# Kernel optimization log

Hardware: AMD Instinct MI355X
Metric: run time of the kernel (lower is better)

## Reference

```python
import math
import jax, jax.numpy as jnp
import numpy as np

B, T, D, NH = 4, 2048, 1024, 16
HS = D // NH
N_BUCKETS = 32
MAX_DIST = 128


def _relative_position_bucket(rp):
    # bidirectional T5 bucketing, n_buckets=32, max_distance=128
    nb = N_BUCKETS // 2  # 16
    buckets = (rp > 0).astype(jnp.int32) * nb
    rp = jnp.abs(rp)
    max_exact = nb // 2  # 8
    is_small = rp < max_exact
    me = max_exact - 1   # 7
    nbm = nb - 1         # 15
    rp_safe = jnp.maximum(rp, 1).astype(jnp.float32)
    rp_large = me + (jnp.log(rp_safe / me) / math.log(MAX_DIST / me) * (nbm - me)).astype(jnp.int32)
    rp_large = jnp.minimum(rp_large, nbm)
    buckets = buckets + jnp.where(is_small, rp, rp_large)
    return buckets


def compute_bias(rel_emb, qT, kT):
    ctx = jnp.arange(qT, dtype=jnp.int32)[:, None]
    mem = jnp.arange(kT, dtype=jnp.int32)[None, :]
    bucket = _relative_position_bucket(mem - ctx)  # [qT, kT]
    values = rel_emb[bucket]                        # [qT, kT, NH]
    return jnp.transpose(values, (2, 0, 1))[None]   # [1, NH, qT, kT]


def setup_inputs() -> dict:
    key = jax.random.key(0)
    ks = jax.random.split(key, 6)
    s = 0.02
    return {
        "queries": jax.random.normal(ks[0], (B, T, D), jnp.float32),
        "Wq": jax.random.normal(ks[1], (D, D), jnp.float32) * s,
        "Wk": jax.random.normal(ks[2], (D, D), jnp.float32) * s,
        "Wv": jax.random.normal(ks[3], (D, D), jnp.float32) * s,
        "Wo": jax.random.normal(ks[4], (D, D), jnp.float32) * s,
        "rel_emb": jax.random.normal(ks[5], (N_BUCKETS, NH), jnp.float32) * s,
    }


def reference(queries, Wq, Wk, Wv, Wo, rel_emb):
    b, t, d = queries.shape
    def split_heads(x):
        return jnp.transpose(x.reshape(b, t, NH, HS), (0, 2, 1, 3))  # [B, nh, T, hs]
    q = split_heads(queries @ Wq.T)
    k = split_heads(queries @ Wk.T)
    v = split_heads(queries @ Wv.T)
    att = jnp.einsum('bhqd,bhkd->bhqk', q, k) * (1.0 / math.sqrt(HS))
    att = att + compute_bias(rel_emb, t, t)
    att = jax.nn.softmax(att, axis=-1)
    o = jnp.einsum('bhqk,bhkd->bhqd', att, v)
    o = jnp.transpose(o, (0, 2, 1, 3)).reshape(b, t, d)
    return o @ Wo.T
```

## Files before the change

kernel.cpp:

```cpp
#include <hip/hip_runtime.h>

#define T_SEQ 2048
#define D_MODEL 1024
#define NHEADS 16
#define HSZ 64
#define BATCH 4

typedef __bf16 bf16x8 __attribute__((ext_vector_type(8)));
typedef float f32x4 __attribute__((ext_vector_type(4)));

__device__ __forceinline__ unsigned short f2bf(float f) {
    unsigned int u = __builtin_bit_cast(unsigned int, f);
    u += 0x7fff + ((u >> 16) & 1);
    return (unsigned short)(u >> 16);
}

__device__ __forceinline__ unsigned int pk2bf(float a, float b) {
#if __has_builtin(__builtin_amdgcn_cvt_pk_bf16_f32)
    typedef __bf16 bf16x2_t __attribute__((ext_vector_type(2)));
    bf16x2_t v = __builtin_amdgcn_cvt_pk_bf16_f32(a, b);
    return __builtin_bit_cast(unsigned int, v);
#else
    return (unsigned int)f2bf(a) | ((unsigned int)f2bf(b) << 16);
#endif
}

__device__ __forceinline__ void gld_lds16(const void* g, void* lds) {
    __builtin_amdgcn_global_load_lds(
        (const __attribute__((address_space(1))) unsigned int*)g,
        (__attribute__((address_space(3))) unsigned int*)lds, 16, 0, 0);
}

__device__ __forceinline__ bf16x8 ld8(const unsigned short* p) {
    return *(const bf16x8*)p;
}

__global__ void cast_x(const float* __restrict__ src, unsigned short* __restrict__ dst, int n4) {
    int i = blockIdx.x * blockDim.x + threadIdx.x;
    if (i >= n4) return;
    float4 v = ((const float4*)src)[i];
    ushort4 o;
    o.x = f2bf(v.x); o.y = f2bf(v.y); o.z = f2bf(v.z); o.w = f2bf(v.w);
    ((ushort4*)dst)[i] = o;
}

__global__ void cast_w(const float* __restrict__ w0, const float* __restrict__ w1,
                       const float* __restrict__ w2, const float* __restrict__ w3,
                       unsigned short* __restrict__ dst) {
    const float* srcs[4] = {w0, w1, w2, w3};
    int wsel = blockIdx.y;
    const float4* src = (const float4*)srcs[wsel];
    int i = blockIdx.x * blockDim.x + threadIdx.x;
    float4 v = src[i];
    ushort4 o;
    o.x = f2bf(v.x); o.y = f2bf(v.y); o.z = f2bf(v.z); o.w = f2bf(v.w);
    ((ushort4*)(dst + (size_t)wsel * 1048576))[i] = o;
}

__global__ void bias_table(const float* __restrict__ rel_emb, float* __restrict__ bias_tab) {
    int idx = blockIdx.x * blockDim.x + threadIdx.x;
    if (idx >= NHEADS * 4095) return;
    int h = idx / 4095;
    int rp = (idx % 4095) - 2047;
    int bucket = rp > 0 ? 16 : 0;
    int arp = rp < 0 ? -rp : rp;
    if (arp < 8) {
        bucket += arp;
    } else {
        float f = logf((float)arp / 7.0f) * (8.0f / logf(128.0f / 7.0f));
        int rl = 7 + (int)f;
        bucket += rl < 15 ? rl : 15;
    }
    bias_tab[idx] = rel_emb[bucket * NHEADS + h] * 1.4426950408889634f;
}

template<int MODE>
__global__ __launch_bounds__(256, 2) void gemm_bt(
    const unsigned short* __restrict__ A,
    const unsigned short* __restrict__ Bw,
    void* __restrict__ out)
{
    constexpr int K = 1024;
    __shared__ unsigned short As[128 * 64];
    __shared__ unsigned short Bs[128 * 64];

    const int tid  = threadIdx.x;
    const int wave = tid >> 6;
    const int lane = tid & 63;
    const int quad = lane >> 4;
    const int l16  = lane & 15;
    const int wm   = wave >> 1;
    const int wn   = wave & 1;
    const int bn   = blockIdx.x;
    const int bm   = blockIdx.y;

    const int r_in = lane >> 3;
    const int lc   = (lane & 7) ^ r_in;

    f32x4 acc[4][4];
    #pragma unroll
    for (int m = 0; m < 4; ++m)
        #pragma unroll
        for (int n = 0; n < 4; ++n)
            acc[m][n] = f32x4{0.f, 0.f, 0.f, 0.f};

    const long a_row0 = (long)bm * 128;
    const long b_row0 = (long)bn * 128;

    for (int kt = 0; kt < K / 64; ++kt) {
        __syncthreads();
        const int k0 = kt * 64 + lc * 8;
        #pragma unroll
        for (int c = 0; c < 4; ++c) {
            int cc = wave * 4 + c;
            int r  = cc * 8 + r_in;
            gld_lds16(A  + (a_row0 + r) * K + k0, &As[cc * 512]);
            gld_lds16(Bw + (b_row0 + r) * K + k0, &Bs[cc * 512]);
        }
        __syncthreads();

        bf16x8 af[4][2], bf[4][2];
        #pragma unroll
        for (int m = 0; m < 4; ++m)
            #pragma unroll
            for (int ks = 0; ks < 2; ++ks) {
                int r  = wm * 64 + m * 16 + l16;
                int pc = (ks * 4 + quad) ^ (r & 7);
                af[m][ks] = ld8(&As[r * 64 + pc * 8]);
            }
        #pragma unroll
        for (int n = 0; n < 4; ++n)
            #pragma unroll
            for (int ks = 0; ks < 2; ++ks) {
                int r  = wn * 64 + n * 16 + l16;
                int pc = (ks * 4 + quad) ^ (r & 7);
                bf[n][ks] = ld8(&Bs[r * 64 + pc * 8]);
            }
        #pragma unroll
        for (int ks = 0; ks < 2; ++ks)
            #pragma unroll
            for (int m = 0; m < 4; ++m)
                #pragma unroll
                for (int n = 0; n < 4; ++n)
                    acc[m][n] = __builtin_amdgcn_mfma_f32_16x16x32_bf16(
                        af[m][ks], bf[n][ks], acc[m][n], 0, 0, 0);
    }

    const int which = (MODE == 4) ? (bn >> 3) : 0;
    #pragma unroll
    for (int m = 0; m < 4; ++m) {
        int row = bm * 128 + wm * 64 + m * 16 + quad * 4;
        #pragma unroll
        for (int n = 0; n < 4; ++n) {
            int col = bn * 128 + wn * 64 + n * 16 + l16;
            if (MODE == 3) {
                float* O = (float*)out;
                #pragma unroll
                for (int r = 0; r < 4; ++r)
                    O[(long)(row + r) * 1024 + col] = acc[m][n][r];
            } else {
                int cl = col & 1023;
                int h = cl >> 6, hs = cl & 63;
                int b = row >> 11, t = row & 2047;
                unsigned short* O = (unsigned short*)out + (size_t)which * 8388608;
                if (which == 2) {
                    ushort4 pk;
                    pk.x = f2bf(acc[m][n][0]); pk.y = f2bf(acc[m][n][1]);
                    pk.z = f2bf(acc[m][n][2]); pk.w = f2bf(acc[m][n][3]);
                    *(ushort4*)&O[(long)((b * 16 + h) * 64 + hs) * 2048 + t] = pk;
                } else {
                    #pragma unroll
                    for (int r = 0; r < 4; ++r) {
                        float v = acc[m][n][r];
                        if (which == 0) v *= 0.125f * 1.4426950408889634f;
                        O[(long)((b * 16 + h) * 2048 + (t + r)) * 64 + hs] = f2bf(v);
                    }
                }
            }
        }
    }
}

__global__ __launch_bounds__(256, 2) void attn(
    const unsigned short* __restrict__ Q,
    const unsigned short* __restrict__ Kb,
    const unsigned short* __restrict__ Vt,
    const float* __restrict__ bias_tab,
    unsigned short* __restrict__ AO)
{
    __shared__ unsigned short Ks[64 * 64];
    __shared__ unsigned short Vs[64 * 64];
    __shared__ unsigned short Ps[256 * 72];
    __shared__ float Bb[2303];

    const int tid  = threadIdx.x;
    const int wave = tid >> 6;
    const int lane = tid & 63;
    const int quad = lane >> 4;
    const int l16  = lane & 15;

    const int bh = blockIdx.y;
    const int b  = bh >> 4, h = bh & 15;
    const int q0 = blockIdx.x * 256;

    const unsigned short* Qg = Q  + (long)bh * T_SEQ * HSZ;
    const unsigned short* Kg = Kb + (long)bh * T_SEQ * HSZ;
    const unsigned short* Vg = Vt + (long)bh * HSZ * T_SEQ;

    {
        const float* bt = bias_tab + h * 4095 + (1792 - q0);
        for (int i = tid; i < 2303; i += 256) Bb[i] = bt[i];
    }

    bf16x8 qf[4][2];
    #pragma unroll
    for (int m = 0; m < 4; ++m)
        #pragma unroll
        for (int ks = 0; ks < 2; ++ks) {
            int t = q0 + wave * 64 + m * 16 + l16;
            qf[m][ks] = ld8(&Qg[(long)t * 64 + ks * 32 + quad * 8]);
        }

    f32x4 o[4][4];
    float li[4][4];
    #pragma unroll
    for (int m = 0; m < 4; ++m) {
        #pragma unroll
        for (int n = 0; n < 4; ++n) o[m][n] = f32x4{0.f, 0.f, 0.f, 0.f};
        #pragma unroll
        for (int r = 0; r < 4; ++r) li[m][r] = 0.0f;
    }

    const int r_in = lane >> 3;
    const int lc   = (lane & 7) ^ r_in;

    for (int kt = 0; kt < T_SEQ / 64; ++kt) {
        __syncthreads();
        #pragma unroll
        for (int c = 0; c < 2; ++c) {
            int cc = wave * 2 + c;
            int r  = cc * 8 + r_in;
            gld_lds16(Kg + (long)(kt * 64 + r) * 64 + lc * 8, &Ks[cc * 512]);
            gld_lds16(Vg + (long)r * T_SEQ + kt * 64 + lc * 8, &Vs[cc * 512]);
        }
        __syncthreads();

        bf16x8 kf[4][2];
        #pragma unroll
        for (int n = 0; n < 4; ++n)
            #pragma unroll
            for (int ks = 0; ks < 2; ++ks) {
                int r  = n * 16 + l16;
                int pc = (ks * 4 + quad) ^ (r & 7);
                kf[n][ks] = ld8(&Ks[r * 64 + pc * 8]);
            }

        #pragma unroll
        for (int m = 0; m < 4; ++m) {
            const int rl   = wave * 64 + m * 16 + quad * 4;
            const int bidx = kt * 64 + l16 - rl + 255;
            #pragma unroll
            for (int n = 0; n < 4; ++n) {
                f32x4 s = f32x4{0.f, 0.f, 0.f, 0.f};
                s = __builtin_amdgcn_mfma_f32_16x16x32_bf16(qf[m][0], kf[n][0], s, 0, 0, 0);
                s = __builtin_amdgcn_mfma_f32_16x16x32_bf16(qf[m][1], kf[n][1], s, 0, 0, 0);
                float p[4];
                #pragma unroll
                for (int r = 0; r < 4; ++r) {
                    p[r] = __builtin_exp2f(s[r] + Bb[bidx + n * 16 - r]);
                    li[m][r] += p[r];
                }
                #pragma unroll
                for (int r = 0; r < 4; r += 2) {
                    unsigned int u = pk2bf(p[r], p[r + 1]);
                    unsigned short* bp = &Ps[(rl + r) * 72 + n * 16 + l16];
                    bp[0]  = (unsigned short)u;
                    bp[72] = (unsigned short)(u >> 16);
                }
            }
        }

        bf16x8 vf[4][2];
        #pragma unroll
        for (int n = 0; n < 4; ++n)
            #pragma unroll
            for (int ks = 0; ks < 2; ++ks) {
                int r  = n * 16 + l16;
                int pc = (ks * 4 + quad) ^ (r & 7);
                vf[n][ks] = ld8(&Vs[r * 64 + pc * 8]);
            }

        asm volatile("s_waitcnt lgkmcnt(0)" ::: "memory");

        #pragma unroll
        for (int m = 0; m < 4; ++m) {
            const unsigned short* pr = &Ps[(wave * 64 + m * 16 + l16) * 72 + quad * 8];
            bf16x8 pf0 = ld8(pr);
            bf16x8 pf1 = ld8(pr + 32);
            #pragma unroll
            for (int n = 0; n < 4; ++n) {
                o[m][n] = __builtin_amdgcn_mfma_f32_16x16x32_bf16(pf0, vf[n][0], o[m][n], 0, 0, 0);
                o[m][n] = __builtin_amdgcn_mfma_f32_16x16x32_bf16(pf1, vf[n][1], o[m][n], 0, 0, 0);
            }
        }
    }

    #pragma unroll
    for (int m = 0; m < 4; ++m)
        #pragma unroll
        for (int st = 1; st < 16; st <<= 1)
            #pragma unroll
            for (int r = 0; r < 4; ++r)
                li[m][r] += __shfl_xor(li[m][r], st);

    #pragma unroll
    for (int m = 0; m < 4; ++m) {
        int trow = q0 + wave * 64 + m * 16 + quad * 4;
        #pragma unroll
        for (int r = 0; r < 4; ++r) {
            float inv = 1.0f / li[m][r];
            #pragma unroll
            for (int n = 0; n < 4; ++n) {
                int col = h * 64 + n * 16 + l16;
                AO[(long)(b * T_SEQ + trow + r) * D_MODEL + col] = f2bf(o[m][n][r] * inv);
            }
        }
    }
}

extern "C" void kernel_launch(void* const* d_in, const int* in_sizes, int n_in,
                              void* d_out, int out_size, void* d_ws, size_t ws_size,
                              hipStream_t stream) {
    const float* x   = (const float*)d_in[0];
    const float* wq  = (const float*)d_in[1];
    const float* wk  = (const float*)d_in[2];
    const float* wv  = (const float*)d_in[3];
    const float* wo  = (const float*)d_in[4];
    const float* rel = (const float*)d_in[5];

    char* ws = (char*)d_ws;
    unsigned short* Xbf = (unsigned short*)(ws);
    unsigned short* Wbf = (unsigned short*)(ws + (16l << 20));
    unsigned short* Qb  = (unsigned short*)(ws + (24l << 20));
    float*          btb = (float*)(ws + (72l << 20));

    cast_x<<<8192, 256, 0, stream>>>(x, Xbf, 2097152);
    cast_w<<<dim3(1024, 4), 256, 0, stream>>>(wq, wk, wv, wo, Wbf);
    bias_table<<<256, 256, 0, stream>>>(rel, btb);

    gemm_bt<4><<<dim3(24, 64), 256, 0, stream>>>(Xbf, Wbf, Qb);

    unsigned short* Kbf = Qb + 8388608;
    unsigned short* Vtb = Qb + 16777216;
    unsigned short* AO  = Xbf;
    attn<<<dim3(8, 64), 256, 0, stream>>>(Qb, Kbf, Vtb, btb, AO);

    gemm_bt<3><<<dim3(8, 64), 256, 0, stream>>>(AO, Wbf + 3 * 1048576, d_out);
}
```

Measured before the change: 325.9 us.

## Compute transposed scores so P stays in registers, skip bias lookup off-band

```diff
diff --git a/kernel.cpp b/kernel.cpp
--- a/kernel.cpp
+++ b/kernel.cpp
@@ -7,6 +7,8 @@
 #define BATCH 4
 
 typedef __bf16 bf16x8 __attribute__((ext_vector_type(8)));
+typedef __bf16 bf16x4 __attribute__((ext_vector_type(4)));
+typedef short short4v __attribute__((ext_vector_type(4)));
 typedef float f32x4 __attribute__((ext_vector_type(4)));
 
 __device__ __forceinline__ unsigned short f2bf(float f) {
@@ -22,6 +24,20 @@
     return __builtin_bit_cast(unsigned int, v);
 #else
     return (unsigned int)f2bf(a) | ((unsigned int)f2bf(b) << 16);
+#endif
+}
+
+__device__ __forceinline__ f32x4 mfma16_bf16(short4v a, short4v b, f32x4 c) {
+#if __has_builtin(__builtin_amdgcn_mfma_f32_16x16x16_bf16)
+    return __builtin_amdgcn_mfma_f32_16x16x16_bf16(
+        __builtin_bit_cast(bf16x4, a), __builtin_bit_cast(bf16x4, b), c, 0, 0, 0);
+#elif __has_builtin(__builtin_amdgcn_mfma_f32_16x16x16bf16_1k)
+    return __builtin_amdgcn_mfma_f32_16x16x16bf16_1k(a, b, c, 0, 0, 0);
+#else
+    f32x4 d;
+    asm volatile("v_mfma_f32_16x16x16_bf16 %0, %1, %2, %3"
+                 : "=v"(d) : "v"(a), "v"(b), "v"(c));
+    return d;
 #endif
 }
 
@@ -188,10 +204,10 @@
     const float* __restrict__ bias_tab,
     unsigned short* __restrict__ AO)
 {
-    __shared__ unsigned short Ks[64 * 64];
-    __shared__ unsigned short Vs[64 * 64];
-    __shared__ unsigned short Ps[256 * 72];
-    __shared__ float Bb[2303];
+    __shared__ __align__(16) char smem[36864];
+    unsigned short* Ks = (unsigned short*)smem;
+    unsigned short* Vs = (unsigned short*)(smem + 8192);
+    float*          Bb = (float*)(smem + 16384);
 
     const int tid  = threadIdx.x;
     const int wave = tid >> 6;
@@ -214,22 +230,25 @@
 
     bf16x8 qf[4][2];
     #pragma unroll
-    for (int m = 0; m < 4; ++m)
+    for (int nt = 0; nt < 4; ++nt)
         #pragma unroll
         for (int ks = 0; ks < 2; ++ks) {
-            int t = q0 + wave * 64 + m * 16 + l16;
-            qf[m][ks] = ld8(&Qg[(long)t * 64 + ks * 32 + quad * 8]);
+            int t = q0 + wave * 64 + nt * 16 + l16;
+            qf[nt][ks] = ld8(&Qg[(long)t * 64 + ks * 32 + quad * 8]);
         }
 
     f32x4 o[4][4];
-    float li[4][4];
-    #pragma unroll
-    for (int m = 0; m < 4; ++m) {
-        #pragma unroll
-        for (int n = 0; n < 4; ++n) o[m][n] = f32x4{0.f, 0.f, 0.f, 0.f};
-        #pragma unroll
-        for (int r = 0; r < 4; ++r) li[m][r] = 0.0f;
-    }
+    float li[4];
+    #pragma unroll
+    for (int mo = 0; mo < 4; ++mo)
+        #pragma unroll
+        for (int nt = 0; nt < 4; ++nt) o[mo][nt] = f32x4{0.f, 0.f, 0.f, 0.f};
+    #pragma unroll
+    for (int nt = 0; nt < 4; ++nt) li[nt] = 0.0f;
+
+    __syncthreads();
+    const float cneg = Bb[0];
+    const float cpos = Bb[2302];
 
     const int r_in = lane >> 3;
     const int lc   = (lane & 7) ^ r_in;
@@ -245,86 +264,81 @@
         }
         __syncthreads();
 
-        bf16x8 kf[4][2];
-        #pragma unroll
-        for (int n = 0; n < 4; ++n)
-            #pragma unroll
-            for (int ks = 0; ks < 2; ++ks) {
-                int r  = n * 16 + l16;
-                int pc = (ks * 4 + quad) ^ (r & 7);
-                kf[n][ks] = ld8(&Ks[r * 64 + pc * 8]);
-            }
-
-        #pragma unroll
-        for (int m = 0; m < 4; ++m) {
-            const int rl   = wave * 64 + m * 16 + quad * 4;
-            const int bidx = kt * 64 + l16 - rl + 255;
-            #pragma unroll
-            for (int n = 0; n < 4; ++n) {
+        const int lo = kt * 64 - q0 - 255;
+        const int hi = kt * 64 + 63 - q0;
+        const bool outband = (lo >= 128) || (hi <= -128);
+        const float cb = (lo >= 128) ? cpos : cneg;
+
+        short4v pfrag[4][4];
+        #pragma unroll
+        for (int mt = 0; mt < 4; ++mt) {
+            int rk = mt * 16 + l16;
+            bf16x8 kf0 = ld8(&Ks[rk * 64 + ((quad)     ^ (rk & 7)) * 8]);
+            bf16x8 kf1 = ld8(&Ks[rk * 64 + ((4 + quad) ^ (rk & 7)) * 8]);
+            #pragma unroll
+            for (int nt = 0; nt < 4; ++nt) {
                 f32x4 s = f32x4{0.f, 0.f, 0.f, 0.f};
-                s = __builtin_amdgcn_mfma_f32_16x16x32_bf16(qf[m][0], kf[n][0], s, 0, 0, 0);
-                s = __builtin_amdgcn_mfma_f32_16x16x32_bf16(qf[m][1], kf[n][1], s, 0, 0, 0);
+                s = __builtin_amdgcn_mfma_f32_16x16x32_bf16(kf0, qf[nt][0], s, 0, 0, 0);
+                s = __builtin_amdgcn_mfma_f32_16x16x32_bf16(kf1, qf[nt][1], s, 0, 0, 0);
                 float p[4];
+                if (outband) {
+                    #pragma unroll
+                    for (int r = 0; r < 4; ++r)
+                        p[r] = __builtin_exp2f(s[r] + cb);
+                } else {
+                    int i0 = kt * 64 + mt * 16 + quad * 4
+                           - wave * 64 - nt * 16 - l16 + 255;
+                    #pragma unroll
+                    for (int r = 0; r < 4; ++r)
+                        p[r] = __builtin_exp2f(s[r] + Bb[i0 + r]);
+                }
+                li[nt] += (p[0] + p[1]) + (p[2] + p[3]);
+                uint2 pk = {pk2bf(p[0], p[1]), pk2bf(p[2], p[3])};
+                pfrag[mt][nt] = __builtin_bit_cast(short4v, pk);
+            }
+        }
+
+        #pragma unroll
+        for (int mo = 0; mo < 4; ++mo) {
+            int rv = mo * 16 + l16;
+            #pragma unroll
+            for (int kc = 0; kc < 4; ++kc) {
+                int ch = ((kc * 2 + (quad >> 1)) ^ (rv & 7));
+                short4v vf = *(const short4v*)&Vs[rv * 64 + ch * 8 + (quad & 1) * 4];
                 #pragma unroll
-                for (int r = 0; r < 4; ++r) {
-                    p[r] = __builtin_exp2f(s[r] + Bb[bidx + n * 16 - r]);
-                    li[m][r] += p[r];
-                }
-                #pragma unroll
-                for (int r = 0; r < 4; r += 2) {
-                    unsigned int u = pk2bf(p[r], p[r + 1]);
-                    unsigned short* bp = &Ps[(rl + r) * 72 + n * 16 + l16];
-                    bp[0]  = (unsigned short)u;
-                    bp[72] = (unsigned short)(u >> 16);
-                }
-            }
-        }
-
-        bf16x8 vf[4][2];
-        #pragma unroll
-        for (int n = 0; n < 4; ++n)
-            #pragma unroll
-            for (int ks = 0; ks < 2; ++ks) {
-                int r  = n * 16 + l16;
-                int pc = (ks * 4 + quad) ^ (r & 7);
-                vf[n][ks] = ld8(&Vs[r * 64 + pc * 8]);
-            }
-
-        asm volatile("s_waitcnt lgkmcnt(0)" ::: "memory");
-
-        #pragma unroll
-        for (int m = 0; m < 4; ++m) {
-            const unsigned short* pr = &Ps[(wave * 64 + m * 16 + l16) * 72 + quad * 8];
-            bf16x8 pf0 = ld8(pr);
-            bf16x8 pf1 = ld8(pr + 32);
-            #pragma unroll
-            for (int n = 0; n < 4; ++n) {
-                o[m][n] = __builtin_amdgcn_mfma_f32_16x16x32_bf16(pf0, vf[n][0], o[m][n], 0, 0, 0);
-                o[m][n] = __builtin_amdgcn_mfma_f32_16x16x32_bf16(pf1, vf[n][1], o[m][n], 0, 0, 0);
-            }
-        }
-    }
-
-    #pragma unroll
-    for (int m = 0; m < 4; ++m)
-        #pragma unroll
-        for (int st = 1; st < 16; st <<= 1)
-            #pragma unroll
-            for (int r = 0; r < 4; ++r)
-                li[m][r] += __shfl_xor(li[m][r], st);
-
-    #pragma unroll
-    for (int m = 0; m < 4; ++m) {
-        int trow = q0 + wave * 64 + m * 16 + quad * 4;
-        #pragma unroll
-        for (int r = 0; r < 4; ++r) {
-            float inv = 1.0f / li[m][r];
-            #pragma unroll
-            for (int n = 0; n < 4; ++n) {
-                int col = h * 64 + n * 16 + l16;
-                AO[(long)(b * T_SEQ + trow + r) * D_MODEL + col] = f2bf(o[m][n][r] * inv);
-            }
-        }
+                for (int nt = 0; nt < 4; ++nt)
+                    o[mo][nt] = mfma16_bf16(vf, pfrag[kc][nt], o[mo][nt]);
+            }
+        }
+    }
+
+    #pragma unroll
+    for (int nt = 0; nt < 4; ++nt) {
+        li[nt] += __shfl_xor(li[nt], 16);
+        li[nt] += __shfl_xor(li[nt], 32);
+    }
+    float inv[4];
+    #pragma unroll
+    for (int nt = 0; nt < 4; ++nt) inv[nt] = 1.0f / li[nt];
+
+    __syncthreads();
+    unsigned short* Ew = (unsigned short*)smem + wave * 4608;
+    #pragma unroll
+    for (int mo = 0; mo < 4; ++mo)
+        #pragma unroll
+        for (int nt = 0; nt < 4; ++nt) {
+            uint2 pk = {pk2bf(o[mo][nt][0] * inv[nt], o[mo][nt][1] * inv[nt]),
+                        pk2bf(o[mo][nt][2] * inv[nt], o[mo][nt][3] * inv[nt])};
+            *(uint2*)&Ew[(nt * 16 + l16) * 72 + mo * 16 + quad * 4] = pk;
+        }
+    asm volatile("s_waitcnt lgkmcnt(0)" ::: "memory");
+
+    #pragma unroll
+    for (int rr = 0; rr < 8; ++rr) {
+        int row   = rr * 8 + (lane >> 3);
+        int chunk = lane & 7;
+        uint4 v = *(const uint4*)&Ew[row * 72 + chunk * 8];
+        *(uint4*)&AO[(long)(b * T_SEQ + q0 + wave * 64 + row) * D_MODEL + h * 64 + chunk * 8] = v;
     }
 }
 
```

After: 336.4 us. 1.03x slower.
